# Kernel tuning notes

Hardware: AMD Instinct MI355X
Metric: run time of the kernel (lower is better)

The kernel has to match this reference:

```python
import jax, jax.numpy as jnp
import numpy as np

B, KL, XL, DIM, H, PB = 4, 128, 4096, 256, 8, 8
HD = DIM // H
SCALE = HD ** -0.5
N_DIS = 64 + 2


def setup_inputs() -> dict:
    key = jax.random.key(0)
    ks = jax.random.split(key, 10)
    x = jax.random.normal(ks[0], (B, XL, DIM), jnp.float32)
    kernal = jax.random.normal(ks[1], (B, KL, DIM), jnp.float32)
    rd = jax.random.randint(ks[2], (B, KL, XL), 0, N_DIS)
    polar_pos = jax.random.randint(ks[3], (B, KL, XL), 0, PB)
    att_mask = jax.random.uniform(ks[4], (B, H, XL, KL)) < 0.1
    W_qkv = jax.random.normal(ks[5], (DIM, 3 * DIM), jnp.float32) * 0.02
    dis_embed = jax.random.normal(ks[6], (N_DIS, H), jnp.float32) * 0.02
    polar_emb = jax.random.normal(ks[7], (PB, 1), jnp.float32) * 0.02
    W_proj = jax.random.normal(ks[8], (DIM, DIM), jnp.float32) * 0.02
    b_proj = jnp.zeros((DIM,), jnp.float32)
    return dict(x=x, kernal=kernal, rd=rd, polar_pos=polar_pos, att_mask=att_mask,
                W_qkv=W_qkv, dis_embed=dis_embed, polar_emb=polar_emb,
                W_proj=W_proj, b_proj=b_proj)


def _heads(t, h):
    b, n, d = t.shape
    return t.reshape(b, n, h, d // h).transpose(0, 2, 1, 3)  # b h n hd


def reference(x, kernal, rd, polar_pos, att_mask, W_qkv, dis_embed, polar_emb, W_proj, b_proj):
    b, xl, dim = x.shape
    kl = kernal.shape[1]
    h = H
    scale = (dim // h) ** -0.5

    q, k, v = [_heads(t, h) for t in jnp.split(x @ W_qkv, 3, axis=-1)]        # b h xl hd
    k_q, k_k, k_v = [_heads(t, h) for t in jnp.split(kernal @ W_qkv, 3, axis=-1)]  # b h kl hd

    rd_e = dis_embed[rd].transpose(0, 3, 1, 2)  # (b,kl,xl,h) -> (b,h,kl,xl)

    # kernel -> x attention scores
    k_x_attn = jnp.einsum('bhkd,bhxd->bhkx', k_q, k) * scale  # b h kl xl

    # main orientation: one-hot-weighted |attn| reduced over x, argmax over polar bins
    pp = jnp.broadcast_to(polar_pos[:, None], (b, h, kl, xl))  # b h kl xl
    polar_hot = jax.nn.one_hot(pp, PB, dtype=k_x_attn.dtype)   # b h kl xl o
    ori_sum = jnp.einsum('bhkx,bhkxo->bhko', jnp.abs(k_x_attn), polar_hot)
    main_ori = jnp.argmax(ori_sum, axis=-1)                    # b h kl
    new_polar = pp - main_ori[..., None]
    new_polar = jnp.where(new_polar < 0, new_polar + PB, new_polar)
    polar_bias = polar_emb[new_polar, 0]                       # b h kl xl

    mask_k = att_mask.transpose(0, 1, 3, 2)                    # b h kl xl
    k_x_attn = jnp.where(mask_k, jnp.asarray(-1e6, k_x_attn.dtype), k_x_attn)
    attn_k = jax.nn.softmax(k_x_attn + rd_e + polar_bias, axis=-1)
    k_out = jnp.einsum('bhkx,bhxd->bhkd', attn_k, v)
    k_out = k_out.transpose(0, 2, 1, 3).reshape(b, kl, dim) @ W_proj + b_proj

    # x -> kernel attention scores
    x_k_attn = jnp.einsum('bhxd,bhkd->bhxk', q, k_k) * scale   # b h xl kl
    x_k_attn = jnp.where(att_mask, jnp.asarray(-1e9, x_k_attn.dtype), x_k_attn)
    x_k_attn = jax.nn.softmax(x_k_attn + rd_e.transpose(0, 1, 3, 2)
                              + polar_bias.transpose(0, 1, 3, 2), axis=-1)
    x_out = jnp.einsum('bhxk,bhkd->bhxd', x_k_attn, k_v)
    x_out = x_out.transpose(0, 2, 1, 3).reshape(b, xl, dim) @ W_proj + b_proj

    return (x_out, k_out)
```

## Files before the change

### kernel.cpp

```cpp
#include <hip/hip_runtime.h>
#include <hip/hip_bf16.h>

#define B_    4
#define KL_   128
#define XL_   4096
#define DIM_  256
#define H_    8
#define HD_   32
#define PB_   8
#define NDIS_ 66
#define TDIM_ 768
#define SCALE_ 0.17677669529663687f
#define NS_   4
#define XCH_  (XL_ / NS_)
#define NCH2_ 64
#define KC2_  16
#define GM_PITCH_ 133

#define NB_CVT_  4096
#define NB_PACK_ 2048
#define NB_WQ_   768
#define NB_WP_   256

typedef float v4f __attribute__((ext_vector_type(4)));
typedef short v8s __attribute__((ext_vector_type(8)));

__device__ __forceinline__ unsigned short f2bf(float f) {
    __hip_bfloat16 h = __float2bfloat16(f);
    return __builtin_bit_cast(unsigned short, h);
}
__device__ __forceinline__ float bf2f(unsigned short u) {
    return __bfloat162float(__builtin_bit_cast(__hip_bfloat16, u));
}
__device__ __forceinline__ void cvt_hilo(float v, unsigned short& hi, unsigned short& lo) {
    hi = f2bf(v);
    lo = f2bf(v - bf2f(hi));
}

__global__ __launch_bounds__(256) void preamble(const float* __restrict__ x,
                                                const int* __restrict__ att_mask,
                                                const float* __restrict__ W_qkv,
                                                const float* __restrict__ W_proj,
                                                unsigned short* __restrict__ xh,
                                                unsigned short* __restrict__ xl,
                                                unsigned int* __restrict__ mbits,
                                                unsigned short* __restrict__ wqh,
                                                unsigned short* __restrict__ wql,
                                                unsigned short* __restrict__ wph,
                                                unsigned short* __restrict__ wpl) {
    const int bid = blockIdx.x, tid = threadIdx.x;
    if (bid < NB_CVT_) {
        size_t i = (size_t)bid * 256 + tid;
        float4 v = *(const float4*)&x[i * 4];
        ushort4 h, l;
        cvt_hilo(v.x, h.x, l.x);
        cvt_hilo(v.y, h.y, l.y);
        cvt_hilo(v.z, h.z, l.z);
        cvt_hilo(v.w, h.w, l.w);
        *(ushort4*)&xh[i * 4] = h;
        *(ushort4*)&xl[i * 4] = l;
    } else if (bid < NB_CVT_ + NB_PACK_) {
        size_t wid = (size_t)(bid - NB_CVT_) * 256 + tid;
        const int* src = &att_mask[wid * 32];
        unsigned bits = 0;
#pragma unroll
        for (int i = 0; i < 8; ++i) {
            int4 m4 = *(const int4*)&src[i * 4];
            bits |= (m4.x ? 1u : 0u) << (i * 4 + 0);
            bits |= (m4.y ? 1u : 0u) << (i * 4 + 1);
            bits |= (m4.z ? 1u : 0u) << (i * 4 + 2);
            bits |= (m4.w ? 1u : 0u) << (i * 4 + 3);
        }
        mbits[wid] = bits;
    } else if (bid < NB_CVT_ + NB_PACK_ + NB_WQ_) {
        int n = bid - (NB_CVT_ + NB_PACK_), k = tid;
        float v = W_qkv[(size_t)k * TDIM_ + n];
        unsigned short h, l;
        cvt_hilo(v, h, l);
        wqh[(size_t)n * DIM_ + k] = h;
        wql[(size_t)n * DIM_ + k] = l;
    } else {
        int n = bid - (NB_CVT_ + NB_PACK_ + NB_WQ_), k = tid;
        float v = W_proj[(size_t)k * DIM_ + n];
        unsigned short h, l;
        cvt_hilo(v, h, l);
        wph[(size_t)n * DIM_ + k] = h;
        wpl[(size_t)n * DIM_ + k] = l;
    }
}

__global__ __launch_bounds__(256) void gemm_out(const unsigned short* __restrict__ Ah,
                                                const unsigned short* __restrict__ Al,
                                                const unsigned short* __restrict__ Bh,
                                                const unsigned short* __restrict__ Bl,
                                                float* __restrict__ C,
                                                const float* __restrict__ bias,
                                                int M, int N, int K) {
    __shared__ __align__(16) unsigned short Ah_s[128 * 32];
    __shared__ __align__(16) unsigned short Al_s[128 * 32];
    __shared__ __align__(16) unsigned short Bh_s[128 * 32];
    __shared__ __align__(16) unsigned short Bl_s[128 * 32];
    const int tid = threadIdx.x;
    const int w = tid >> 6, lane = tid & 63;
    const int c = lane & 15, q = lane >> 4;

    const int NBX = N >> 7;
    const int id = blockIdx.x;
    const int xcd = id & 7, grp = id >> 3;
    const int bm = ((grp / NBX) * 8 + xcd) * 128;
    const int bn = (grp % NBX) * 128;

    const int lrow = lane >> 2;
    const int lcol = (lane & 3) * 8;

    v4f acc[2][8] = {};
    for (int k0 = 0; k0 < K; k0 += 32) {
        __syncthreads();
#pragma unroll
        for (int i = 0; i < 2; ++i) {
            const int chunk = w * 2 + i;
            const int row = chunk * 16 + lrow;
            const size_t ga = (size_t)(bm + row) * K + k0 + lcol;
            const size_t gb = (size_t)(bn + row) * K + k0 + lcol;
            const int lo = chunk * 512;
            __builtin_amdgcn_global_load_lds(
                (const __attribute__((address_space(1))) unsigned int*)&Ah[ga],
                (__attribute__((address_space(3))) unsigned int*)&Ah_s[lo], 16, 0, 0);
            __builtin_amdgcn_global_load_lds(
                (const __attribute__((address_space(1))) unsigned int*)&Al[ga],
                (__attribute__((address_space(3))) unsigned int*)&Al_s[lo], 16, 0, 0);
            __builtin_amdgcn_global_load_lds(
                (const __attribute__((address_space(1))) unsigned int*)&Bh[gb],
                (__attribute__((address_space(3))) unsigned int*)&Bh_s[lo], 16, 0, 0);
            __builtin_amdgcn_global_load_lds(
                (const __attribute__((address_space(1))) unsigned int*)&Bl[gb],
                (__attribute__((address_space(3))) unsigned int*)&Bl_s[lo], 16, 0, 0);
        }
        asm volatile("s_waitcnt vmcnt(0)" ::: "memory");
        __syncthreads();
        v8s afh[2], afl[2];
#pragma unroll
        for (int mt = 0; mt < 2; ++mt) {
            afh[mt] = *(v8s*)&Ah_s[(w * 32 + mt * 16 + c) * 32 + q * 8];
            afl[mt] = *(v8s*)&Al_s[(w * 32 + mt * 16 + c) * 32 + q * 8];
        }
#pragma unroll
        for (int nt = 0; nt < 8; ++nt) {
            v8s bfh = *(v8s*)&Bh_s[(nt * 16 + c) * 32 + q * 8];
            v8s bfl = *(v8s*)&Bl_s[(nt * 16 + c) * 32 + q * 8];
#pragma unroll
            for (int mt = 0; mt < 2; ++mt) {
                acc[mt][nt] = __builtin_amdgcn_mfma_f32_16x16x32_bf16(afl[mt], bfh, acc[mt][nt], 0, 0, 0);
                acc[mt][nt] = __builtin_amdgcn_mfma_f32_16x16x32_bf16(afh[mt], bfl, acc[mt][nt], 0, 0, 0);
                acc[mt][nt] = __builtin_amdgcn_mfma_f32_16x16x32_bf16(afh[mt], bfh, acc[mt][nt], 0, 0, 0);
            }
        }
    }
#pragma unroll
    for (int mt = 0; mt < 2; ++mt) {
#pragma unroll
        for (int nt = 0; nt < 8; ++nt) {
            int col = bn + nt * 16 + c;
            float bv = bias ? bias[col] : 0.0f;
#pragma unroll
            for (int r = 0; r < 4; ++r) {
                int row = bm + w * 32 + mt * 16 + q * 4 + r;
                C[(size_t)row * N + col] = acc[mt][nt][r] + bv;
            }
        }
    }
}

__global__ __launch_bounds__(256) void gemm_qkv(const unsigned short* __restrict__ Ah,
                                                const unsigned short* __restrict__ Al,
                                                const unsigned short* __restrict__ Bh,
                                                const unsigned short* __restrict__ Bl,
                                                int M, int N, int K,
                                                unsigned short* __restrict__ qh,
                                                unsigned short* __restrict__ kh,
                                                unsigned short* __restrict__ kl2,
                                                float* __restrict__ vx) {
    __shared__ __align__(16) char SMEM[64 * GM_PITCH_ * 4];
    unsigned short* Ah_s = (unsigned short*)SMEM;
    unsigned short* Al_s = Ah_s + 4096;
    unsigned short* Bh_s = Ah_s + 8192;
    unsigned short* Bl_s = Ah_s + 12288;
    float* scratch = (float*)SMEM;

    const int tid = threadIdx.x;
    const int w = tid >> 6, lane = tid & 63;
    const int c = lane & 15, q = lane >> 4;

    const int NBX = N >> 7;
    const int id = blockIdx.x;
    const int xcd = id & 7, grp = id >> 3;
    const int bm = ((grp / NBX) * 8 + xcd) * 128;
    const int bn = (grp % NBX) * 128;

    const int lrow = lane >> 2;
    const int lcol = (lane & 3) * 8;

    v4f acc[2][8] = {};
    for (int k0 = 0; k0 < K; k0 += 32) {
        __syncthreads();
#pragma unroll
        for (int i = 0; i < 2; ++i) {
            const int chunk = w * 2 + i;
            const int row = chunk * 16 + lrow;
            const size_t ga = (size_t)(bm + row) * K + k0 + lcol;
            const size_t gb = (size_t)(bn + row) * K + k0 + lcol;
            const int lo = chunk * 512;
            __builtin_amdgcn_global_load_lds(
                (const __attribute__((address_space(1))) unsigned int*)&Ah[ga],
                (__attribute__((address_space(3))) unsigned int*)&Ah_s[lo], 16, 0, 0);
            __builtin_amdgcn_global_load_lds(
                (const __attribute__((address_space(1))) unsigned int*)&Al[ga],
                (__attribute__((address_space(3))) unsigned int*)&Al_s[lo], 16, 0, 0);
            __builtin_amdgcn_global_load_lds(
                (const __attribute__((address_space(1))) unsigned int*)&Bh[gb],
                (__attribute__((address_space(3))) unsigned int*)&Bh_s[lo], 16, 0, 0);
            __builtin_amdgcn_global_load_lds(
                (const __attribute__((address_space(1))) unsigned int*)&Bl[gb],
                (__attribute__((address_space(3))) unsigned int*)&Bl_s[lo], 16, 0, 0);
        }
        asm volatile("s_waitcnt vmcnt(0)" ::: "memory");
        __syncthreads();
        v8s afh[2], afl[2];
#pragma unroll
        for (int mt = 0; mt < 2; ++mt) {
            afh[mt] = *(v8s*)&Ah_s[(w * 32 + mt * 16 + c) * 32 + q * 8];
            afl[mt] = *(v8s*)&Al_s[(w * 32 + mt * 16 + c) * 32 + q * 8];
        }
#pragma unroll
        for (int nt = 0; nt < 8; ++nt) {
            v8s bfh = *(v8s*)&Bh_s[(nt * 16 + c) * 32 + q * 8];
            v8s bfl = *(v8s*)&Bl_s[(nt * 16 + c) * 32 + q * 8];
#pragma unroll
            for (int mt = 0; mt < 2; ++mt) {
                acc[mt][nt] = __builtin_amdgcn_mfma_f32_16x16x32_bf16(afl[mt], bfh, acc[mt][nt], 0, 0, 0);
                acc[mt][nt] = __builtin_amdgcn_mfma_f32_16x16x32_bf16(afh[mt], bfl, acc[mt][nt], 0, 0, 0);
                acc[mt][nt] = __builtin_amdgcn_mfma_f32_16x16x32_bf16(afh[mt], bfh, acc[mt][nt], 0, 0, 0);
            }
        }
    }
    if (bn >= 2 * DIM_) {
#pragma unroll
        for (int mt = 0; mt < 2; ++mt) {
#pragma unroll
            for (int nt = 0; nt < 8; ++nt) {
                int col = bn + nt * 16 + c - 2 * DIM_;
#pragma unroll
                for (int r = 0; r < 4; ++r) {
                    int row = bm + w * 32 + mt * 16 + q * 4 + r;
                    vx[(size_t)row * DIM_ + col] = acc[mt][nt][r];
                }
            }
        }
    } else {
        for (int mt = 0; mt < 2; ++mt) {
            __syncthreads();
#pragma unroll
            for (int nt = 0; nt < 8; ++nt)
#pragma unroll
                for (int r = 0; r < 4; ++r)
                    scratch[(w * 16 + q * 4 + r) * GM_PITCH_ + nt * 16 + c] = acc[mt][nt][r];
            __syncthreads();
            const int or_ = tid & 63, oc = (tid >> 6) * 32;
            const int grow = bm + (or_ >> 4) * 32 + mt * 16 + (or_ & 15);
            const float* src = &scratch[or_ * GM_PITCH_ + oc];
            if (bn < DIM_) {
                unsigned short* dst = &qh[(size_t)grow * DIM_ + bn + oc];
#pragma unroll
                for (int j4 = 0; j4 < 4; ++j4) {
                    unsigned short tmp[8];
#pragma unroll
                    for (int j = 0; j < 8; ++j) tmp[j] = f2bf(src[j4 * 8 + j]);
                    *(uint4*)&dst[j4 * 8] = *(uint4*)&tmp[0];
                }
            } else {
                const size_t o = (size_t)grow * DIM_ + bn - DIM_ + oc;
#pragma unroll
                for (int j4 = 0; j4 < 4; ++j4) {
                    unsigned short th[8], tl[8];
#pragma unroll
                    for (int j = 0; j < 8; ++j) cvt_hilo(src[j4 * 8 + j], th[j], tl[j]);
                    *(uint4*)&kh[o + j4 * 8] = *(uint4*)&th[0];
                    *(uint4*)&kl2[o + j4 * 8] = *(uint4*)&tl[0];
                }
            }
        }
    }
}

__global__ __launch_bounds__(256) void gemm64(const float* __restrict__ A,
                                              const float* __restrict__ Bw,
                                              float* __restrict__ C,
                                              const float* __restrict__ bias,
                                              int M, int N, int K) {
    __shared__ __align__(16) float As[16][68];
    __shared__ __align__(16) float Bs[16][64];
    const int tid = threadIdx.x;
    const int tx = tid & 15, ty = tid >> 4;
    const int bn = blockIdx.x * 64, bm = blockIdx.y * 64;
    const int am = tid >> 2, ac = tid & 3;
    float acc[4][4] = {};
    for (int k0 = 0; k0 < K; k0 += 16) {
        float4 a4 = *(const float4*)&A[(size_t)(bm + am) * K + k0 + ac * 4];
        As[ac * 4 + 0][am] = a4.x;
        As[ac * 4 + 1][am] = a4.y;
        As[ac * 4 + 2][am] = a4.z;
        As[ac * 4 + 3][am] = a4.w;
        *(float4*)&Bs[ty][tx * 4] = *(const float4*)&Bw[(size_t)(k0 + ty) * N + bn + tx * 4];
        __syncthreads();
#pragma unroll
        for (int kk = 0; kk < 16; ++kk) {
            float4 av = *(const float4*)&As[kk][ty * 4];
            float4 bv = *(const float4*)&Bs[kk][tx * 4];
            float a[4] = {av.x, av.y, av.z, av.w};
            float b[4] = {bv.x, bv.y, bv.z, bv.w};
#pragma unroll
            for (int i = 0; i < 4; ++i)
#pragma unroll
                for (int j = 0; j < 4; ++j) acc[i][j] += a[i] * b[j];
        }
        __syncthreads();
    }
#pragma unroll
    for (int i = 0; i < 4; ++i) {
        int m = bm + ty * 4 + i;
#pragma unroll
        for (int j = 0; j < 4; ++j) {
            int n = bn + tx * 4 + j;
            float v = acc[i][j];
            if (bias) v += bias[n];
            C[(size_t)m * N + n] = v;
        }
    }
}

__global__ __launch_bounds__(256) void gemm64_qkv(const float* __restrict__ A,
                                                  const float* __restrict__ Bw,
                                                  unsigned short* __restrict__ Kqh,
                                                  unsigned short* __restrict__ Kql,
                                                  unsigned short* __restrict__ Kk_bf,
                                                  unsigned short* __restrict__ VT_bf,
                                                  int M, int N, int K) {
    __shared__ __align__(16) float As[16][68];
    __shared__ __align__(16) float Bs[16][64];
    const int tid = threadIdx.x;
    const int tx = tid & 15, ty = tid >> 4;
    const int bn = blockIdx.x * 64, bm = blockIdx.y * 64;
    const int am = tid >> 2, ac = tid & 3;
    float acc[4][4] = {};
    for (int k0 = 0; k0 < K; k0 += 16) {
        float4 a4 = *(const float4*)&A[(size_t)(bm + am) * K + k0 + ac * 4];
        As[ac * 4 + 0][am] = a4.x;
        As[ac * 4 + 1][am] = a4.y;
        As[ac * 4 + 2][am] = a4.z;
        As[ac * 4 + 3][am] = a4.w;
        *(float4*)&Bs[ty][tx * 4] = *(const float4*)&Bw[(size_t)(k0 + ty) * N + bn + tx * 4];
        __syncthreads();
#pragma unroll
        for (int kk = 0; kk < 16; ++kk) {
            float4 av = *(const float4*)&As[kk][ty * 4];
            float4 bv = *(const float4*)&Bs[kk][tx * 4];
            float a[4] = {av.x, av.y, av.z, av.w};
            float b[4] = {bv.x, bv.y, bv.z, bv.w};
#pragma unroll
            for (int i = 0; i < 4; ++i)
#pragma unroll
                for (int j = 0; j < 4; ++j) acc[i][j] += a[i] * b[j];
        }
        __syncthreads();
    }
#pragma unroll
    for (int i = 0; i < 4; ++i) {
        int m = bm + ty * 4 + i;
        int b = m >> 7, k = m & 127;
#pragma unroll
        for (int j = 0; j < 4; ++j) {
            int n = bn + tx * 4 + j;
            float v = acc[i][j];
            if (n < DIM_) {
                unsigned short hi, lo;
                cvt_hilo(v, hi, lo);
                int h = n >> 5, d = n & 31;
                size_t o = ((size_t)(b * H_ + h) * KL_ + k) * HD_ + d;
                Kqh[o] = hi;
                Kql[o] = lo;
            } else if (n < 2 * DIM_) {
                int nn = n - DIM_, h = nn >> 5, d = nn & 31;
                Kk_bf[((size_t)(b * H_ + h) * KL_ + k) * HD_ + d] = f2bf(v);
            } else {
                int nn = n - 2 * DIM_, h = nn >> 5, d = nn & 31;
                VT_bf[((size_t)(b * H_ + h) * HD_ + d) * KL_ + k] = f2bf(v);
            }
        }
    }
}

__global__ __launch_bounds__(256) void score_bins_mfma4(const unsigned short* __restrict__ kxh,
                                                        const unsigned short* __restrict__ kxl,
                                                        const unsigned short* __restrict__ Kqh_g,
                                                        const unsigned short* __restrict__ Kql_g,
                                                        const int* __restrict__ rd,
                                                        const int* __restrict__ polar_pos,
                                                        const unsigned int* __restrict__ mbits,
                                                        const float* __restrict__ dis_embed,
                                                        __hip_bfloat16* __restrict__ Sg,
                                                        float* __restrict__ binspart) {
    const int b = blockIdx.z, h = blockIdx.y, xc = blockIdx.x;
    const int x0 = xc * 64;
    const int tid = threadIdx.x;
    const int w = tid >> 6, lane = tid & 63;
    const int c15 = lane & 15, q = lane >> 4;
    const size_t bh = (size_t)(b * H_ + h);

    __shared__ unsigned int mskb[64][5];
    __shared__ float de_h[NDIS_];
    __shared__ float binsL[8][4][16][PB_ + 1];
    __shared__ __align__(16) unsigned short Ss[2][16][72];

    {
        int xr = tid >> 2, kg = tid & 3;
        mskb[xr][kg] = mbits[(bh * XL_ + x0 + xr) * 4 + kg];
    }
    if (tid < NDIS_) de_h[tid] = dis_embed[tid * H_ + h];
    __syncthreads();

    v8s axh, axl;
    {
        const size_t aoff = ((size_t)b * XL_ + x0 + w * 16 + c15) * DIM_ + h * HD_ + q * 8;
        axh = *(const v8s*)&kxh[aoff];
        axl = *(const v8s*)&kxl[aoff];
    }

    v8s bqh[2], bql[2];
    int4 r4[2], p4[2];
    auto load_nt = [&](int nt, int s) {
        const int k = nt * 16 + c15;
        const size_t kqoff = (bh * KL_ + k) * HD_ + q * 8;
        bqh[s] = *(const v8s*)&Kqh_g[kqoff];
        bql[s] = *(const v8s*)&Kql_g[kqoff];
        const size_t rowoff = ((size_t)(b * KL_ + k)) * XL_ + x0 + w * 16 + q * 4;
        r4[s] = *(const int4*)&rd[rowoff];
        p4[s] = *(const int4*)&polar_pos[rowoff];
    };
    load_nt(0, 0);

#pragma unroll
    for (int nt = 0; nt < 8; ++nt) {
        const int s = nt & 1;
        if (nt < 7) load_nt(nt + 1, s ^ 1);

        const int k = nt * 16 + c15;
        v4f D = {0.f, 0.f, 0.f, 0.f};
        D = __builtin_amdgcn_mfma_f32_16x16x32_bf16(axl, bqh[s], D, 0, 0, 0);
        D = __builtin_amdgcn_mfma_f32_16x16x32_bf16(axh, bql[s], D, 0, 0, 0);
        D = __builtin_amdgcn_mfma_f32_16x16x32_bf16(axh, bqh[s], D, 0, 0, 0);

        float bins[PB_] = {};
        {
            int rv[4] = {r4[s].x, r4[s].y, r4[s].z, r4[s].w};
            int pv[4] = {p4[s].x, p4[s].y, p4[s].z, p4[s].w};
            ushort4 pack;
#pragma unroll
            for (int r = 0; r < 4; ++r) {
                float sc = D[r] * SCALE_;
                float a = fabsf(sc);
                int pp = pv[r];
#pragma unroll
                for (int pb = 0; pb < PB_; ++pb) bins[pb] += (pp == pb) ? a : 0.0f;
                int xloc = w * 16 + q * 4 + r;
                int mbit = (mskb[xloc][k >> 5] >> (k & 31)) & 1;
                float sp = (mbit ? -1e6f : sc) + de_h[rv[r]];
                ((unsigned short*)&pack)[r] = f2bf(sp);
            }
            *(ushort4*)&Ss[s][c15][w * 16 + q * 4] = pack;
        }

#pragma unroll
        for (int pb = 0; pb < PB_; ++pb) {
            bins[pb] += __shfl_xor(bins[pb], 16);
            bins[pb] += __shfl_xor(bins[pb], 32);
        }
        if (q == 0) {
#pragma unroll
            for (int pb = 0; pb < PB_; ++pb) binsL[nt][w][c15][pb] = bins[pb];
        }

        __syncthreads();
        {
            int row = tid >> 4, seg = tid & 15;
            unsigned short* dst = (unsigned short*)Sg +
                (bh * KL_ + nt * 16 + row) * XL_ + x0 + seg * 4;
            *(uint2*)dst = *(const uint2*)&Ss[s][row][seg * 4];
        }
    }
    __syncthreads();
    {
        int k = tid >> 1, half = tid & 1;
        int nt = k >> 4, c = k & 15;
        float4 s = {0.f, 0.f, 0.f, 0.f};
#pragma unroll
        for (int w4 = 0; w4 < 4; ++w4) {
            const float* bp = &binsL[nt][w4][c][half * 4];
            s.x += bp[0]; s.y += bp[1]; s.z += bp[2]; s.w += bp[3];
        }
        *(float4*)&binspart[(bh * KL_ + k) * (NCH2_ * PB_) + xc * PB_ + half * 4] = s;
    }
}

__global__ __launch_bounds__(256) void bins_argmax(const float* __restrict__ binspart,
                                                   int* __restrict__ main_ori) {
    const int w = threadIdx.x >> 6, lane = threadIdx.x & 63;
    const int row = blockIdx.x * 4 + w;
    float s[PB_];
#pragma unroll
    for (int pb = 0; pb < PB_; ++pb) s[pb] = 0.0f;
    if (lane < NCH2_) {
        const float* bp = &binspart[(size_t)row * (NCH2_ * PB_) + lane * PB_];
#pragma unroll
        for (int pb = 0; pb < PB_; ++pb) s[pb] = bp[pb];
    }
#pragma unroll
    for (int m = 1; m < 64; m <<= 1)
#pragma unroll
        for (int pb = 0; pb < PB_; ++pb) s[pb] += __shfl_xor(s[pb], m);
    if (lane == 0) {
        float best = s[0];
        int bi = 0;
#pragma unroll
        for (int pb = 1; pb < PB_; ++pb)
            if (s[pb] > best) { best = s[pb]; bi = pb; }
        main_ori[row] = bi;
    }
}

__global__ __launch_bounds__(256) void flash_cached2(const float* __restrict__ vx,
                                                     const __hip_bfloat16* __restrict__ Sg,
                                                     const int* __restrict__ polar_pos,
                                                     const float* __restrict__ polar_emb,
                                                     const int* __restrict__ main_ori,
                                                     float* __restrict__ part) {
    const int b = blockIdx.z, h = blockIdx.y;
    const int kch = blockIdx.x / NS_, xc = blockIdx.x % NS_;
    const int k0 = kch * KC2_;
    const int tid = threadIdx.x;
    const int ki = tid >> 4, xt = tid & 15;

    __shared__ __align__(16) float4 vs[64][9];
    __shared__ int pol_s[KC2_][68];
    __shared__ float pe[PB_];

    if (tid < PB_) pe[tid] = polar_emb[tid];
    const size_t bh = (size_t)(b * H_ + h);
    const size_t row_k = bh * KL_ + k0 + ki;
    const int mo = main_ori[row_k];
    const int xbeg = xc * XCH_;

    float l = 0.f;
    float4 acc[8] = {};
    __syncthreads();
    for (int t = 0; t < XCH_ / 64; ++t) {
        const int x0 = xbeg + t * 64;
        __syncthreads();
#pragma unroll
        for (int i = 0; i < 2; ++i) {
            int id = tid + 256 * i;
            int row = id >> 3, c = id & 7;
            vs[row][c] = *(const float4*)&vx[(size_t)(b * XL_ + x0 + row) * DIM_ + h * HD_ + c * 4];
        }
        {
            int kk = tid >> 4, c = tid & 15;
            *(int4*)&pol_s[kk][c * 4] =
                *(const int4*)&polar_pos[(size_t)(b * KL_ + k0 + kk) * XL_ + x0 + c * 4];
        }
        __syncthreads();
#pragma unroll
        for (int j = 0; j < 4; ++j) {
            int xl = xt + 16 * j;
            int x = x0 + xl;
            float sp = __bfloat162float(Sg[row_k * XL_ + x]);
            int pp = pol_s[ki][xl];
            int np = pp - mo;
            np += (np >> 31) & PB_;
            float p = __expf(sp + pe[np]);
            l += p;
#pragma unroll
            for (int c = 0; c < 8; ++c) {
                float4 v = vs[xl][c];
                acc[c].x += p * v.x; acc[c].y += p * v.y;
                acc[c].z += p * v.z; acc[c].w += p * v.w;
            }
        }
    }
#pragma unroll
    for (int m = 1; m < 16; m <<= 1) {
        l += __shfl_xor(l, m, 16);
#pragma unroll
        for (int c = 0; c < 8; ++c) {
            acc[c].x += __shfl_xor(acc[c].x, m, 16);
            acc[c].y += __shfl_xor(acc[c].y, m, 16);
            acc[c].z += __shfl_xor(acc[c].z, m, 16);
            acc[c].w += __shfl_xor(acc[c].w, m, 16);
        }
    }
    if (xt == 0) {
        float* dst = &part[(size_t)(row_k * NS_ + xc) * 36];
#pragma unroll
        for (int c = 0; c < 8; ++c) *(float4*)&dst[c * 4] = acc[c];
        dst[32] = l;
    }
}

__global__ __launch_bounds__(256) void merge_cached(const float* __restrict__ part,
                                                    float* __restrict__ kout_pre) {
    const int tid = threadIdx.x;
    const int ri = tid >> 5, d = tid & 31;
    const int row = blockIdx.x * 8 + ri;
    float l = 0.f, a = 0.f;
#pragma unroll
    for (int c = 0; c < NS_; ++c) {
        const float* p = &part[(size_t)(row * NS_ + c) * 36];
        l += p[32];
        a += p[d];
    }
    int k = row & (KL_ - 1);
    int bh = row >> 7;
    int h = bh & (H_ - 1), b = bh >> 3;
    kout_pre[(size_t)(b * KL_ + k) * DIM_ + h * HD_ + d] = a / l;
}

__global__ __launch_bounds__(256) void attn_x_mfma(const unsigned short* __restrict__ qxh,
                                                   const unsigned short* __restrict__ Kk_bf,
                                                   const unsigned short* __restrict__ VT_bf,
                                                   const int* __restrict__ rd,
                                                   const int* __restrict__ polar_pos,
                                                   const unsigned int* __restrict__ mbits,
                                                   const float* __restrict__ dis_embed,
                                                   const float* __restrict__ polar_emb,
                                                   const int* __restrict__ main_ori,
                                                   unsigned short* __restrict__ oh,
                                                   unsigned short* __restrict__ ol) {
    const int b = blockIdx.z, h = blockIdx.y;
    const int x0 = blockIdx.x * 64;
    const int tid = threadIdx.x;
    const int wave = tid >> 6, lane = tid & 63;
    const int c = lane & 15, q = lane >> 4;

    __shared__ __align__(16) unsigned short P_s[4][16][136];
    __shared__ unsigned short rp_s[KL_][72];
    __shared__ unsigned int msk_s[64][5];
    __shared__ float de_h[NDIS_];
    __shared__ float pe[PB_];
    __shared__ int mo_s[KL_];

    const size_t bh = (size_t)(b * H_ + h);
    if (tid < NDIS_) de_h[tid] = dis_embed[tid * H_ + h];
    if (tid < PB_) pe[tid] = polar_emb[tid];
    if (tid < KL_) mo_s[tid] = main_ori[bh * KL_ + tid];
    {
        int xr = tid >> 2, kg = tid & 3;
        msk_s[xr][kg] = mbits[(bh * XL_ + x0 + xr) * 4 + kg];
    }
    __syncthreads();

#pragma unroll
    for (int i = 0; i < 8; ++i) {
        int id = tid + 256 * i;
        int k = id >> 4, cc = id & 15;
        size_t gb = (size_t)(b * KL_ + k) * XL_ + x0 + cc * 4;
        int4 r4 = *(const int4*)&rd[gb];
        int4 p4 = *(const int4*)&polar_pos[gb];
        int mo = mo_s[k];
        int n0 = p4.x - mo; n0 += (n0 >> 31) & PB_;
        int n1 = p4.y - mo; n1 += (n1 >> 31) & PB_;
        int n2 = p4.z - mo; n2 += (n2 >> 31) & PB_;
        int n3 = p4.w - mo; n3 += (n3 >> 31) & PB_;
        rp_s[k][cc * 4 + 0] = (unsigned short)(r4.x | (n0 << 8));
        rp_s[k][cc * 4 + 1] = (unsigned short)(r4.y | (n1 << 8));
        rp_s[k][cc * 4 + 2] = (unsigned short)(r4.z | (n2 << 8));
        rp_s[k][cc * 4 + 3] = (unsigned short)(r4.w | (n3 << 8));
    }
    __syncthreads();

    v8s aq = *(const v8s*)&qxh[(size_t)(b * XL_ + x0 + wave * 16 + c) * DIM_ + h * HD_ + q * 8];

    const unsigned short* KkB = &Kk_bf[(size_t)bh * KL_ * HD_];
    v4f S[8];
#pragma unroll
    for (int t = 0; t < 8; ++t) {
        v8s bk = *(const v8s*)&KkB[(size_t)(t * 16 + c) * HD_ + q * 8];
        S[t] = __builtin_amdgcn_mfma_f32_16x16x32_bf16(aq, bk, (v4f){0.f, 0.f, 0.f, 0.f}, 0, 0, 0);
    }

    const int xloc = wave * 16;
    float lr[4] = {0.f, 0.f, 0.f, 0.f};
#pragma unroll
    for (int t = 0; t < 8; ++t) {
#pragma unroll
        for (int r = 0; r < 4; ++r) {
            int krow = t * 16 + c;
            int xrow = q * 4 + r;
            unsigned short rp = rp_s[krow][xloc + xrow];
            int mbit = (msk_s[xloc + xrow][krow >> 5] >> (krow & 31)) & 1;
            float sval = S[t][r] * SCALE_;
            float tval = (mbit ? -25.0f : sval) + de_h[rp & 0x7f] + pe[(rp >> 8) & 7];
            float p = __expf(tval);
            unsigned short pb = f2bf(p);
            P_s[wave][xrow][krow] = pb;
            lr[r] += bf2f(pb);
        }
    }
#pragma unroll
    for (int r = 0; r < 4; ++r) {
#pragma unroll
        for (int m = 1; m < 16; m <<= 1) lr[r] += __shfl_xor(lr[r], m);
    }
    __syncthreads();

    const unsigned short* VTB = &VT_bf[(size_t)bh * HD_ * KL_];
    v4f O0 = {0.f, 0.f, 0.f, 0.f}, O1 = {0.f, 0.f, 0.f, 0.f};
#pragma unroll
    for (int kc = 0; kc < 4; ++kc) {
        v8s ap = *(v8s*)&P_s[wave][c][kc * 32 + q * 8];
        v8s bv0 = *(const v8s*)&VTB[(size_t)c * KL_ + kc * 32 + q * 8];
        v8s bv1 = *(const v8s*)&VTB[(size_t)(16 + c) * KL_ + kc * 32 + q * 8];
        O0 = __builtin_amdgcn_mfma_f32_16x16x32_bf16(ap, bv0, O0, 0, 0, 0);
        O1 = __builtin_amdgcn_mfma_f32_16x16x32_bf16(ap, bv1, O1, 0, 0, 0);
    }

#pragma unroll
    for (int r = 0; r < 4; ++r) {
        int xg = x0 + wave * 16 + q * 4 + r;
        float inv = 1.0f / lr[r];
        size_t obase = (size_t)(b * XL_ + xg) * DIM_ + h * HD_;
        float v0 = O0[r] * inv;
        float v1 = O1[r] * inv;
        unsigned short h0, l0, h1, l1;
        cvt_hilo(v0, h0, l0);
        cvt_hilo(v1, h1, l1);
        oh[obase + c] = h0;
        ol[obase + c] = l0;
        oh[obase + 16 + c] = h1;
        ol[obase + 16 + c] = l1;
    }
}

extern "C" void kernel_launch(void* const* d_in, const int* in_sizes, int n_in,
                              void* d_out, int out_size, void* d_ws, size_t ws_size,
                              hipStream_t stream) {
    const float* x         = (const float*)d_in[0];
    const float* kernal    = (const float*)d_in[1];
    const int* rd          = (const int*)d_in[2];
    const int* polar_pos   = (const int*)d_in[3];
    const int* att_mask    = (const int*)d_in[4];
    const float* W_qkv     = (const float*)d_in[5];
    const float* dis_embed = (const float*)d_in[6];
    const float* polar_emb = (const float*)d_in[7];
    const float* W_proj    = (const float*)d_in[8];
    const float* b_proj    = (const float*)d_in[9];
    float* out             = (float*)d_out;

    char* base = (char*)d_ws;
    size_t off = 0;
    auto alloc = [&](size_t bytes) { void* p = base + off; off = (off + bytes + 255) & ~255ULL; return p; };
    const size_t MX = (size_t)B_ * XL_;

    float* vx        = (float*)alloc(MX * DIM_ * 4);
    unsigned short* qxh = (unsigned short*)alloc(MX * DIM_ * 2);
    unsigned short* kxh = (unsigned short*)alloc(MX * DIM_ * 2);
    unsigned short* kxl = (unsigned short*)alloc(MX * DIM_ * 2);
    float* binspart  = (float*)alloc((size_t)B_ * H_ * KL_ * NCH2_ * PB_ * 4);
    float* kout_pre  = (float*)alloc((size_t)B_ * KL_ * DIM_ * 4);
    int* main_ori    = (int*)alloc(B_ * H_ * KL_ * 4);
    float* part      = (float*)alloc((size_t)B_ * H_ * KL_ * NS_ * 36 * 4);
    __hip_bfloat16* Sg = (__hip_bfloat16*)alloc((size_t)B_ * H_ * KL_ * XL_ * 2);
    unsigned short* wph = (unsigned short*)alloc((size_t)DIM_ * DIM_ * 2);
    unsigned short* wpl = (unsigned short*)alloc((size_t)DIM_ * DIM_ * 2);
    unsigned short* wqh = (unsigned short*)alloc((size_t)TDIM_ * DIM_ * 2);
    unsigned short* wql = (unsigned short*)alloc((size_t)TDIM_ * DIM_ * 2);
    unsigned int* mbits = (unsigned int*)alloc((size_t)B_ * H_ * XL_ * (KL_ / 32) * 4);
    unsigned short* Kqh_g = (unsigned short*)alloc((size_t)B_ * H_ * KL_ * HD_ * 2);
    unsigned short* Kql_g = (unsigned short*)alloc((size_t)B_ * H_ * KL_ * HD_ * 2);
    unsigned short* Kk_bf = (unsigned short*)alloc((size_t)B_ * H_ * KL_ * HD_ * 2);
    unsigned short* VT_bf = (unsigned short*)alloc((size_t)B_ * H_ * HD_ * KL_ * 2);

    unsigned short* xh = (unsigned short*)Sg;
    unsigned short* xl_ = xh + MX * DIM_;
    unsigned short* oh = (unsigned short*)Sg;
    unsigned short* ol = oh + MX * DIM_;

    preamble<<<dim3(NB_CVT_ + NB_PACK_ + NB_WQ_ + NB_WP_), 256, 0, stream>>>(
        x, att_mask, W_qkv, W_proj, xh, xl_, mbits, wqh, wql, wph, wpl);

    gemm_qkv<<<dim3((TDIM_ / 128) * (MX / 128)), 256, 0, stream>>>(
        xh, xl_, wqh, wql, MX, TDIM_, DIM_, qxh, kxh, kxl, vx);
    gemm64_qkv<<<dim3(TDIM_ / 64, (B_ * KL_) / 64), 256, 0, stream>>>(
        kernal, W_qkv, Kqh_g, Kql_g, Kk_bf, VT_bf, B_ * KL_, TDIM_, DIM_);

    score_bins_mfma4<<<dim3(NCH2_, H_, B_), 256, 0, stream>>>(
        kxh, kxl, Kqh_g, Kql_g, rd, polar_pos, mbits, dis_embed, Sg, binspart);
    bins_argmax<<<dim3(B_ * H_ * KL_ / 4), 256, 0, stream>>>(binspart, main_ori);
    flash_cached2<<<dim3((KL_ / KC2_) * NS_, H_, B_), 256, 0, stream>>>(
        vx, Sg, polar_pos, polar_emb, main_ori, part);
    merge_cached<<<dim3(B_ * H_ * KL_ / 8), 256, 0, stream>>>(part, kout_pre);

    attn_x_mfma<<<dim3(XL_ / 64, H_, B_), 256, 0, stream>>>(
        qxh, Kk_bf, VT_bf, rd, polar_pos, mbits, dis_embed, polar_emb, main_ori, oh, ol);

    gemm_out<<<dim3((DIM_ / 128) * (MX / 128)), 256, 0, stream>>>(
        oh, ol, wph, wpl, out, b_proj, MX, DIM_, DIM_);
    gemm64<<<dim3(DIM_ / 64, (B_ * KL_) / 64), 256, 0, stream>>>(
        kout_pre, W_proj, out + (size_t)B_ * XL_ * DIM_, b_proj, B_ * KL_, DIM_, DIM_);
}
```

Measured before the change: 330.2 us.

## Move kernel-side P·V to MFMA with bf16 transposed V and packed polar bins

Replaces the scalar-FMA flash_cached2 kernel with flash_mfma, which turns the exponentiated scores into bf16 and runs P·V on MFMA 16x16x32 instructions. The QKV GEMM epilogue now writes V as a transposed bf16 layout (b,h,d,x) in place of fp32 row-major. The preamble packs polar_pos into 4-bit nibbles so the flash kernel reads one eighth of the bytes. The x-split is raised from 4 to 32 chunks, which enlarges the partial buffer the merge has to reduce. The price is lower precision from bf16 probabilities and bf16 V, plus scattered 8-byte transposed stores in the GEMM epilogue.

```diff
diff --git a/kernel.cpp b/kernel.cpp
--- a/kernel.cpp
+++ b/kernel.cpp
@@ -11,16 +11,17 @@
 #define NDIS_ 66
 #define TDIM_ 768
 #define SCALE_ 0.17677669529663687f
-#define NS_   4
-#define XCH_  (XL_ / NS_)
 #define NCH2_ 64
 #define KC2_  16
+#define NS2_  32
+#define XC2_  (XL_ / NS2_)
 #define GM_PITCH_ 133
 
 #define NB_CVT_  4096
 #define NB_PACK_ 2048
 #define NB_WQ_   768
 #define NB_WP_   256
+#define NB_PP_   1024
 
 typedef float v4f __attribute__((ext_vector_type(4)));
 typedef short v8s __attribute__((ext_vector_type(8)));
@@ -41,13 +42,15 @@
                                                 const int* __restrict__ att_mask,
                                                 const float* __restrict__ W_qkv,
                                                 const float* __restrict__ W_proj,
+                                                const int* __restrict__ polar_pos,
                                                 unsigned short* __restrict__ xh,
                                                 unsigned short* __restrict__ xl,
                                                 unsigned int* __restrict__ mbits,
                                                 unsigned short* __restrict__ wqh,
                                                 unsigned short* __restrict__ wql,
                                                 unsigned short* __restrict__ wph,
-                                                unsigned short* __restrict__ wpl) {
+                                                unsigned short* __restrict__ wpl,
+                                                unsigned int* __restrict__ pp4) {
     const int bid = blockIdx.x, tid = threadIdx.x;
     if (bid < NB_CVT_) {
         size_t i = (size_t)bid * 256 + tid;
@@ -79,13 +82,23 @@
         cvt_hilo(v, h, l);
         wqh[(size_t)n * DIM_ + k] = h;
         wql[(size_t)n * DIM_ + k] = l;
-    } else {
+    } else if (bid < NB_CVT_ + NB_PACK_ + NB_WQ_ + NB_WP_) {
         int n = bid - (NB_CVT_ + NB_PACK_ + NB_WQ_), k = tid;
         float v = W_proj[(size_t)k * DIM_ + n];
         unsigned short h, l;
         cvt_hilo(v, h, l);
         wph[(size_t)n * DIM_ + k] = h;
         wpl[(size_t)n * DIM_ + k] = l;
+    } else {
+        size_t wid = (size_t)(bid - (NB_CVT_ + NB_PACK_ + NB_WQ_ + NB_WP_)) * 256 + tid;
+        const int* src = &polar_pos[wid * 8];
+        int4 a = *(const int4*)&src[0];
+        int4 b4 = *(const int4*)&src[4];
+        unsigned pk = (unsigned)(a.x & 7) | ((unsigned)(a.y & 7) << 4) |
+                      ((unsigned)(a.z & 7) << 8) | ((unsigned)(a.w & 7) << 12) |
+                      ((unsigned)(b4.x & 7) << 16) | ((unsigned)(b4.y & 7) << 20) |
+                      ((unsigned)(b4.z & 7) << 24) | ((unsigned)(b4.w & 7) << 28);
+        pp4[wid] = pk;
     }
 }
 
@@ -179,7 +192,7 @@
                                                 unsigned short* __restrict__ qh,
                                                 unsigned short* __restrict__ kh,
                                                 unsigned short* __restrict__ kl2,
-                                                float* __restrict__ vx) {
+                                                unsigned short* __restrict__ VTx) {
     __shared__ __align__(16) char SMEM[64 * GM_PITCH_ * 4];
     unsigned short* Ah_s = (unsigned short*)SMEM;
     unsigned short* Al_s = Ah_s + 4096;
@@ -248,12 +261,14 @@
         for (int mt = 0; mt < 2; ++mt) {
 #pragma unroll
             for (int nt = 0; nt < 8; ++nt) {
-                int col = bn + nt * 16 + c - 2 * DIM_;
-#pragma unroll
-                for (int r = 0; r < 4; ++r) {
-                    int row = bm + w * 32 + mt * 16 + q * 4 + r;
-                    vx[(size_t)row * DIM_ + col] = acc[mt][nt][r];
-                }
+                int nn = bn + nt * 16 + c - 2 * DIM_;
+                int h = nn >> 5, d = nn & 31;
+                int row0 = bm + w * 32 + mt * 16 + q * 4;
+                int b = row0 >> 12, x = row0 & (XL_ - 1);
+                unsigned short t4[4];
+#pragma unroll
+                for (int r = 0; r < 4; ++r) t4[r] = f2bf(acc[mt][nt][r]);
+                *(ushort4*)&VTx[((size_t)(b * H_ + h) * HD_ + d) * XL_ + x] = *(ushort4*)&t4[0];
             }
         }
     } else {
@@ -537,80 +552,79 @@
     }
 }
 
-__global__ __launch_bounds__(256) void flash_cached2(const float* __restrict__ vx,
-                                                     const __hip_bfloat16* __restrict__ Sg,
-                                                     const int* __restrict__ polar_pos,
-                                                     const float* __restrict__ polar_emb,
-                                                     const int* __restrict__ main_ori,
-                                                     float* __restrict__ part) {
-    const int b = blockIdx.z, h = blockIdx.y;
-    const int kch = blockIdx.x / NS_, xc = blockIdx.x % NS_;
-    const int k0 = kch * KC2_;
+__global__ __launch_bounds__(256) void flash_mfma(const __hip_bfloat16* __restrict__ Sg,
+                                                  const unsigned int* __restrict__ pp4,
+                                                  const unsigned short* __restrict__ VTx,
+                                                  const float* __restrict__ polar_emb,
+                                                  const int* __restrict__ main_ori,
+                                                  float* __restrict__ part) {
+    const int b = blockIdx.z, h = blockIdx.y, xc = blockIdx.x;
     const int tid = threadIdx.x;
-    const int ki = tid >> 4, xt = tid & 15;
-
-    __shared__ __align__(16) float4 vs[64][9];
-    __shared__ int pol_s[KC2_][68];
-    __shared__ float pe[PB_];
-
-    if (tid < PB_) pe[tid] = polar_emb[tid];
+    const int w = tid >> 6, lane = tid & 63;
+    const int c = lane & 15, q = lane >> 4;
     const size_t bh = (size_t)(b * H_ + h);
-    const size_t row_k = bh * KL_ + k0 + ki;
-    const int mo = main_ori[row_k];
-    const int xbeg = xc * XCH_;
-
-    float l = 0.f;
-    float4 acc[8] = {};
+    const int xbeg = xc * XC2_;
+
+    __shared__ int mo_s[KL_];
+    __shared__ float pe_s[PB_];
+    if (tid < KL_) mo_s[tid] = main_ori[bh * KL_ + tid];
+    if (tid < PB_) pe_s[tid] = polar_emb[tid];
     __syncthreads();
-    for (int t = 0; t < XCH_ / 64; ++t) {
-        const int x0 = xbeg + t * 64;
-        __syncthreads();
-#pragma unroll
-        for (int i = 0; i < 2; ++i) {
-            int id = tid + 256 * i;
-            int row = id >> 3, c = id & 7;
-            vs[row][c] = *(const float4*)&vx[(size_t)(b * XL_ + x0 + row) * DIM_ + h * HD_ + c * 4];
-        }
-        {
-            int kk = tid >> 4, c = tid & 15;
-            *(int4*)&pol_s[kk][c * 4] =
-                *(const int4*)&polar_pos[(size_t)(b * KL_ + k0 + kk) * XL_ + x0 + c * 4];
-        }
-        __syncthreads();
-#pragma unroll
-        for (int j = 0; j < 4; ++j) {
-            int xl = xt + 16 * j;
-            int x = x0 + xl;
-            float sp = __bfloat162float(Sg[row_k * XL_ + x]);
-            int pp = pol_s[ki][xl];
-            int np = pp - mo;
-            np += (np >> 31) & PB_;
-            float p = __expf(sp + pe[np]);
-            l += p;
-#pragma unroll
-            for (int c = 0; c < 8; ++c) {
-                float4 v = vs[xl][c];
-                acc[c].x += p * v.x; acc[c].y += p * v.y;
-                acc[c].z += p * v.z; acc[c].w += p * v.w;
+
+    const int wk0 = w * 32;
+    const int mo[2] = {mo_s[wk0 + c], mo_s[wk0 + 16 + c]};
+    const unsigned short* SgU = (const unsigned short*)Sg;
+
+    v4f acc[2][2] = {};
+    float lsum[2] = {0.f, 0.f};
+
+    for (int s = 0; s < XC2_ / 32; ++s) {
+        const int xs = xbeg + s * 32;
+        v8s pa[2];
+#pragma unroll
+        for (int kt = 0; kt < 2; ++kt) {
+            const int k = wk0 + kt * 16 + c;
+            v8s sv = *(const v8s*)&SgU[(bh * KL_ + k) * XL_ + xs + q * 8];
+            unsigned pw = pp4[((size_t)(b * KL_ + k)) * (XL_ / 8) + (xs >> 3) + q];
+            unsigned short pk[8];
+#pragma unroll
+            for (int j = 0; j < 8; ++j) {
+                float sp = bf2f((unsigned short)sv[j]);
+                int np = (((int)(pw >> (j * 4)) & 7) - mo[kt]) & 7;
+                float p = __expf(sp + pe_s[np]);
+                unsigned short pb = f2bf(p);
+                pk[j] = pb;
+                lsum[kt] += bf2f(pb);
             }
-        }
-    }
-#pragma unroll
-    for (int m = 1; m < 16; m <<= 1) {
-        l += __shfl_xor(l, m, 16);
-#pragma unroll
-        for (int c = 0; c < 8; ++c) {
-            acc[c].x += __shfl_xor(acc[c].x, m, 16);
-            acc[c].y += __shfl_xor(acc[c].y, m, 16);
-            acc[c].z += __shfl_xor(acc[c].z, m, 16);
-            acc[c].w += __shfl_xor(acc[c].w, m, 16);
-        }
-    }
-    if (xt == 0) {
-        float* dst = &part[(size_t)(row_k * NS_ + xc) * 36];
-#pragma unroll
-        for (int c = 0; c < 8; ++c) *(float4*)&dst[c * 4] = acc[c];
-        dst[32] = l;
+            pa[kt] = *(v8s*)pk;
+        }
+#pragma unroll
+        for (int dt = 0; dt < 2; ++dt) {
+            v8s bv = *(const v8s*)&VTx[((size_t)bh * HD_ + dt * 16 + c) * XL_ + xs + q * 8];
+            acc[0][dt] = __builtin_amdgcn_mfma_f32_16x16x32_bf16(pa[0], bv, acc[0][dt], 0, 0, 0);
+            acc[1][dt] = __builtin_amdgcn_mfma_f32_16x16x32_bf16(pa[1], bv, acc[1][dt], 0, 0, 0);
+        }
+    }
+
+#pragma unroll
+    for (int kt = 0; kt < 2; ++kt) {
+        lsum[kt] += __shfl_xor(lsum[kt], 16);
+        lsum[kt] += __shfl_xor(lsum[kt], 32);
+    }
+#pragma unroll
+    for (int kt = 0; kt < 2; ++kt) {
+#pragma unroll
+        for (int dt = 0; dt < 2; ++dt) {
+#pragma unroll
+            for (int r = 0; r < 4; ++r) {
+                int krow = wk0 + kt * 16 + q * 4 + r;
+                part[((size_t)(bh * KL_ + krow) * NS2_ + xc) * 36 + dt * 16 + c] = acc[kt][dt][r];
+            }
+        }
+        if (q == 0) {
+            int krow = wk0 + kt * 16 + c;
+            part[((size_t)(bh * KL_ + krow) * NS2_ + xc) * 36 + 32] = lsum[kt];
+        }
     }
 }
 
@@ -620,9 +634,9 @@
     const int ri = tid >> 5, d = tid & 31;
     const int row = blockIdx.x * 8 + ri;
     float l = 0.f, a = 0.f;
-#pragma unroll
-    for (int c = 0; c < NS_; ++c) {
-        const float* p = &part[(size_t)(row * NS_ + c) * 36];
+#pragma unroll 4
+    for (int c = 0; c < NS2_; ++c) {
+        const float* p = &part[((size_t)row * NS2_ + c) * 36];
         l += p[32];
         a += p[d];
     }
@@ -768,20 +782,21 @@
     auto alloc = [&](size_t bytes) { void* p = base + off; off = (off + bytes + 255) & ~255ULL; return p; };
     const size_t MX = (size_t)B_ * XL_;
 
-    float* vx        = (float*)alloc(MX * DIM_ * 4);
+    unsigned short* VTx = (unsigned short*)alloc((size_t)B_ * H_ * HD_ * XL_ * 2);
     unsigned short* qxh = (unsigned short*)alloc(MX * DIM_ * 2);
     unsigned short* kxh = (unsigned short*)alloc(MX * DIM_ * 2);
     unsigned short* kxl = (unsigned short*)alloc(MX * DIM_ * 2);
     float* binspart  = (float*)alloc((size_t)B_ * H_ * KL_ * NCH2_ * PB_ * 4);
     float* kout_pre  = (float*)alloc((size_t)B_ * KL_ * DIM_ * 4);
     int* main_ori    = (int*)alloc(B_ * H_ * KL_ * 4);
-    float* part      = (float*)alloc((size_t)B_ * H_ * KL_ * NS_ * 36 * 4);
+    float* part      = (float*)alloc((size_t)B_ * H_ * KL_ * NS2_ * 36 * 4);
     __hip_bfloat16* Sg = (__hip_bfloat16*)alloc((size_t)B_ * H_ * KL_ * XL_ * 2);
     unsigned short* wph = (unsigned short*)alloc((size_t)DIM_ * DIM_ * 2);
     unsigned short* wpl = (unsigned short*)alloc((size_t)DIM_ * DIM_ * 2);
     unsigned short* wqh = (unsigned short*)alloc((size_t)TDIM_ * DIM_ * 2);
     unsigned short* wql = (unsigned short*)alloc((size_t)TDIM_ * DIM_ * 2);
     unsigned int* mbits = (unsigned int*)alloc((size_t)B_ * H_ * XL_ * (KL_ / 32) * 4);
+    unsigned int* pp4   = (unsigned int*)alloc((size_t)B_ * KL_ * (XL_ / 8) * 4);
     unsigned short* Kqh_g = (unsigned short*)alloc((size_t)B_ * H_ * KL_ * HD_ * 2);
     unsigned short* Kql_g = (unsigned short*)alloc((size_t)B_ * H_ * KL_ * HD_ * 2);
     unsigned short* Kk_bf = (unsigned short*)alloc((size_t)B_ * H_ * KL_ * HD_ * 2);
@@ -792,19 +807,19 @@
     unsigned short* oh = (unsigned short*)Sg;
     unsigned short* ol = oh + MX * DIM_;
 
-    preamble<<<dim3(NB_CVT_ + NB_PACK_ + NB_WQ_ + NB_WP_), 256, 0, stream>>>(
-        x, att_mask, W_qkv, W_proj, xh, xl_, mbits, wqh, wql, wph, wpl);
+    preamble<<<dim3(NB_CVT_ + NB_PACK_ + NB_WQ_ + NB_WP_ + NB_PP_), 256, 0, stream>>>(
+        x, att_mask, W_qkv, W_proj, polar_pos, xh, xl_, mbits, wqh, wql, wph, wpl, pp4);
 
     gemm_qkv<<<dim3((TDIM_ / 128) * (MX / 128)), 256, 0, stream>>>(
-        xh, xl_, wqh, wql, MX, TDIM_, DIM_, qxh, kxh, kxl, vx);
+        xh, xl_, wqh, wql, MX, TDIM_, DIM_, qxh, kxh, kxl, VTx);
     gemm64_qkv<<<dim3(TDIM_ / 64, (B_ * KL_) / 64), 256, 0, stream>>>(
         kernal, W_qkv, Kqh_g, Kql_g, Kk_bf, VT_bf, B_ * KL_, TDIM_, DIM_);
 
     score_bins_mfma4<<<dim3(NCH2_, H_, B_), 256, 0, stream>>>(
         kxh, kxl, Kqh_g, Kql_g, rd, polar_pos, mbits, dis_embed, Sg, binspart);
     bins_argmax<<<dim3(B_ * H_ * KL_ / 4), 256, 0, stream>>>(binspart, main_ori);
-    flash_cached2<<<dim3((KL_ / KC2_) * NS_, H_, B_), 256, 0, stream>>>(
-        vx, Sg, polar_pos, polar_emb, main_ori, part);
+    flash_mfma<<<dim3(NS2_, H_, B_), 256, 0, stream>>>(
+        Sg, pp4, VTx, polar_emb, main_ori, part);
     merge_cached<<<dim3(B_ * H_ * KL_ / 8), 256, 0, stream>>>(part, kout_pre);
 
     attn_x_mfma<<<dim3(XL_ / 64, H_, B_), 256, 0, stream>>>(
```

After: 321.6 us. -2.6%, faster.
